# Performance work log

Hardware: AMD Instinct MI355X
Metric: run time of the kernel (lower is better)

The kernel has to match this reference:

```python
import jax, jax.numpy as jnp
import numpy as np

NODE_DIM = 128
NUM_IRREPS = 224          # 128 + 64 + 32 gates (one per irrep channel)
SPH_DIM = 480             # 128*1 + 64*3 + 32*5
HIDDEN = NODE_DIM + 2 * NUM_IRREPS  # 576
NUM_BASIS = 20
N_NODES = 10000
N_EDGES = 160000
# Each gate scalar is broadcast over its irrep's (2l+1) components.
_REPEATS = np.array([1] * 128 + [3] * 64 + [5] * 32)


def _expand_gate(g):
    # [E, 224] -> [E, 480], repeating each gate over its irrep dimension
    return jnp.repeat(g, _REPEATS, axis=-1, total_repeat_length=SPH_DIM)


def setup_inputs() -> dict:
    key = jax.random.key(0)
    ks = jax.random.split(key, 12)
    x_scalar = jax.random.normal(ks[0], (N_NODES, NODE_DIM), dtype=jnp.float32)
    x_spherical = jax.random.normal(ks[1], (N_NODES, SPH_DIM), dtype=jnp.float32)
    rbf = jax.random.uniform(ks[2], (N_EDGES, NUM_BASIS), dtype=jnp.float32)
    fcut = jax.random.uniform(ks[3], (N_EDGES, 1), dtype=jnp.float32)
    rsh = jax.random.normal(ks[4], (N_EDGES, SPH_DIM), dtype=jnp.float32)
    edge_index = jax.random.randint(ks[5], (2, N_EDGES), 0, N_NODES, dtype=jnp.int64)
    s1 = 1.0 / np.sqrt(NODE_DIM)
    s2 = 1.0 / np.sqrt(NUM_BASIS)
    W1 = jax.random.uniform(ks[6], (NODE_DIM, NODE_DIM), jnp.float32, -s1, s1)
    b1 = jnp.zeros((NODE_DIM,), jnp.float32)
    W2 = jax.random.uniform(ks[7], (NODE_DIM, HIDDEN), jnp.float32, -s1, s1)
    b2 = jnp.zeros((HIDDEN,), jnp.float32)
    Wr = jax.random.uniform(ks[8], (NUM_BASIS, HIDDEN), jnp.float32, -s2, s2)
    br = jnp.zeros((HIDDEN,), jnp.float32)
    return {"x_scalar": x_scalar, "x_spherical": x_spherical, "rbf": rbf,
            "fcut": fcut, "rsh": rsh, "edge_index": edge_index,
            "W1": W1, "b1": b1, "W2": W2, "b2": b2, "Wr": Wr, "br": br}


def reference(x_scalar, x_spherical, rbf, fcut, rsh, edge_index,
              W1, b1, W2, b2, Wr, br):
    src, dst = edge_index[0], edge_index[1]
    # scalar MLP: Linear -> SiLU -> Linear
    scalar_out = jax.nn.silu(x_scalar @ W1 + b1) @ W2 + b2          # [N, 576]
    filter_weight = (rbf @ Wr + br) * fcut                          # [E, 576]
    filter_out = scalar_out[dst] * filter_weight                    # [E, 576]
    gate_state = filter_out[:, :NUM_IRREPS]                         # [E, 224]
    gate_edge = filter_out[:, NUM_IRREPS:2 * NUM_IRREPS]            # [E, 224]
    message_scalar = filter_out[:, 2 * NUM_IRREPS:]                 # [E, 128]
    # ElementwiseTensorProduct(edge_irreps, '224x0e'): per-channel scalar gating
    message_spherical = (x_spherical[dst] * _expand_gate(gate_state)
                         + rsh * _expand_gate(gate_edge))           # [E, 480]
    new_scalar = x_scalar.at[src].add(message_scalar)
    new_spherical = x_spherical.at[src].add(message_spherical)
    return (new_scalar, new_spherical)
```

## Files before the change

kernel.cpp:

```cpp
#include <hip/hip_runtime.h>

#define NODE_DIM 128
#define NUM_IRREPS 224
#define SPH_DIM 480
#define HIDDEN 576
#define NUM_BASIS 20
#define N_NODES 10000
#define N_EDGES 160000
#define NPB 4
#define EB 16
#define NT 36
#define IRP 233
#define SCP 138
#define PREP_BLOCKS 2048
#define MLP_BLOCKS ((N_NODES + NPB - 1) / NPB)

typedef __attribute__((ext_vector_type(8))) short short8v;
typedef __attribute__((ext_vector_type(4))) float f32x4;

__device__ __forceinline__ unsigned short f2bf(float f) {
    unsigned int u = __builtin_bit_cast(unsigned int, f);
    u = (u + 0x7fff + ((u >> 16) & 1)) >> 16;
    return (unsigned short)u;
}
__device__ __forceinline__ float bf2f(unsigned short h) {
    unsigned int u = ((unsigned int)h) << 16;
    return __builtin_bit_cast(float, u);
}

__global__ __launch_bounds__(256) void prep_mlp_kernel(
    const float* __restrict__ xs, const float* __restrict__ xsp,
    float* __restrict__ out,
    const int* __restrict__ eidx, int* __restrict__ counts,
    const float* __restrict__ Wr, unsigned short* __restrict__ bfrag,
    const float* __restrict__ W1, const float* __restrict__ b1,
    const float* __restrict__ W2, const float* __restrict__ b2,
    unsigned short* __restrict__ so_bf)
{
    const int t = threadIdx.x;
    if (blockIdx.x < PREP_BLOCKS) {
        const int stride = PREP_BLOCKS * 256;
        const int gt = blockIdx.x * 256 + t;
        for (int i = gt; i < N_NODES * NODE_DIM; i += stride) out[i] = xs[i];
        float* o2 = out + (size_t)N_NODES * NODE_DIM;
        for (int i = gt; i < N_NODES * SPH_DIM; i += stride) o2[i] = xsp[i];
        if (gt < N_EDGES) atomicAdd(&counts[eidx[gt]], 1);
        if (blockIdx.x == PREP_BLOCKS - 1) {
            for (int idx = t; idx < NT * 64; idx += 256) {
                const int nt = idx >> 6, l = idx & 63;
                const int col = nt * 16 + (l & 15);
                const int kb = (l >> 4) * 8;
                #pragma unroll
                for (int j = 0; j < 8; ++j) {
                    const int k = kb + j;
                    bfrag[(size_t)idx * 8 + j] = (k < NUM_BASIS) ? f2bf(Wr[k * HIDDEN + col]) : (unsigned short)0;
                }
            }
        }
        return;
    }
    __shared__ float xsm[NPB][NODE_DIM];
    __shared__ float hsm[NPB][NODE_DIM];
    const int n0 = (blockIdx.x - PREP_BLOCKS) * NPB;
    const int half = t >> 7;
    const int tc = t & 127;

    #pragma unroll
    for (int i = 0; i < 2; ++i) {
        const int nn = 2 * half + i;
        const int node = n0 + nn;
        xsm[nn][tc] = (node < N_NODES) ? xs[(size_t)node * NODE_DIM + tc] : 0.f;
    }
    __syncthreads();

    float acc[2] = {b1[tc], b1[tc]};
    for (int k = 0; k < NODE_DIM; ++k) {
        const float w = W1[k * NODE_DIM + tc];
        #pragma unroll
        for (int i = 0; i < 2; ++i) acc[i] = fmaf(xsm[2 * half + i][k], w, acc[i]);
    }
    #pragma unroll
    for (int i = 0; i < 2; ++i) {
        const float v = acc[i];
        hsm[2 * half + i][tc] = v / (1.f + __expf(-v));
    }
    __syncthreads();

    for (int j = t; j < HIDDEN; j += 256) {
        float a2[NPB];
        #pragma unroll
        for (int n = 0; n < NPB; ++n) a2[n] = b2[j];
        for (int k = 0; k < NODE_DIM; ++k) {
            const float w = W2[k * HIDDEN + j];
            #pragma unroll
            for (int n = 0; n < NPB; ++n) a2[n] = fmaf(hsm[n][k], w, a2[n]);
        }
        #pragma unroll
        for (int n = 0; n < NPB; ++n) {
            const int node = n0 + n;
            if (node < N_NODES) so_bf[(size_t)node * HIDDEN + j] = f2bf(a2[n]);
        }
    }
}

__global__ __launch_bounds__(1024) void scan_kernel(const int* __restrict__ counts,
                                                    int* __restrict__ offsets,
                                                    int* __restrict__ cursor) {
    __shared__ int wsum[16];
    const int tid = threadIdx.x;
    int vals[10];
    int run = 0;
    #pragma unroll
    for (int i = 0; i < 10; ++i) {
        int idx = tid * 10 + i;
        int c = (idx < N_NODES) ? counts[idx] : 0;
        vals[i] = run;
        run += c;
    }
    const int lane = tid & 63, w = tid >> 6;
    int inc = run;
    #pragma unroll
    for (int off = 1; off < 64; off <<= 1) {
        int v = __shfl_up(inc, off);
        if (lane >= off) inc += v;
    }
    if (lane == 63) wsum[w] = inc;
    __syncthreads();
    if (w == 0) {
        int v = (lane < 16) ? wsum[lane] : 0;
        #pragma unroll
        for (int off = 1; off < 16; off <<= 1) {
            int u = __shfl_up(v, off);
            if (lane >= off) v += u;
        }
        if (lane < 16) wsum[lane] = v;
    }
    __syncthreads();
    const int wbase = (w > 0) ? wsum[w - 1] : 0;
    const int base = wbase + inc - run;
    #pragma unroll
    for (int i = 0; i < 10; ++i) {
        int idx = tid * 10 + i;
        if (idx < N_NODES) {
            int v = base + vals[i];
            offsets[idx] = v;
            cursor[idx] = v;
        }
    }
    if (tid == 1023) offsets[N_NODES] = wbase + inc;
}

__global__ __launch_bounds__(256) void scatter_kernel(const int* __restrict__ eidx,
                                                      int* __restrict__ cursor,
                                                      int* __restrict__ edge_order,
                                                      int* __restrict__ edge_src) {
    int i = blockIdx.x * blockDim.x + threadIdx.x;
    if (i < N_EDGES) {
        int s = eidx[i];
        int pos = atomicAdd(&cursor[s], 1);
        edge_order[pos] = i;
        edge_src[pos] = s;
    }
}

__device__ __forceinline__ int gate_of(int d) {
    return (d < 128) ? d : (d < 320) ? (128 + (d - 128) / 3) : (192 + (d - 320) / 5);
}

__global__ __launch_bounds__(256, 4) void edge_mfma(
    const float* __restrict__ xsp,
    const float* __restrict__ rbf, const float* __restrict__ fcut,
    const float* __restrict__ rsh, const int* __restrict__ eidx,
    const unsigned short* __restrict__ bfrag, const float* __restrict__ br,
    const unsigned short* __restrict__ so_bf,
    const int* __restrict__ edge_order, const int* __restrict__ edge_src,
    float* __restrict__ out_scalar, float* __restrict__ out_sph)
{
    __shared__ unsigned int   pair_s[EB][IRP];
    __shared__ unsigned short scal_s[EB][SCP];
    __shared__ int   e_s[EB];
    __shared__ int   src_s[EB];
    __shared__ int   dst_s[EB];
    __shared__ float fc_s[EB];

    const int t = threadIdx.x;
    const int base = blockIdx.x * EB;
    const int lane = t & 63, w = t >> 6;

    const int m_row = lane & 15;
    const int kb = (lane >> 4) * 8;
    const int e_row = edge_order[base + m_row];
    short8v a0;
    {
        const float* rrow = rbf + (size_t)e_row * NUM_BASIS;
        #pragma unroll
        for (int j = 0; j < 8; ++j) {
            const int k = kb + j;
            a0[j] = (k < NUM_BASIS) ? (short)f2bf(rrow[k]) : (short)0;
        }
    }

    if (t < EB) {
        int pos = base + t;
        int e = edge_order[pos];
        e_s[t]   = e;
        src_s[t] = edge_src[pos];
        dst_s[t] = eidx[N_EDGES + e];
        fc_s[t]  = fcut[e];
    }
    __syncthreads();

    {
        const int rbase = (lane >> 4) * 4;
        int   dA[4];
        float fA[4];
        #pragma unroll
        for (int r = 0; r < 4; ++r) { dA[r] = dst_s[rbase + r]; fA[r] = fc_s[rbase + r]; }
        #pragma unroll
        for (int i = 0; i < NT / 4; ++i) {
            const int nt = w * (NT / 4) + i;
            const short8v bf = *(const short8v*)(bfrag + (size_t)(nt * 64 + lane) * 8);
            f32x4 c0 = {0.f, 0.f, 0.f, 0.f};
            c0 = __builtin_amdgcn_mfma_f32_16x16x32_bf16(a0, bf, c0, 0, 0, 0);
            const int col = nt * 16 + (lane & 15);
            const float brc = br[col];
            #pragma unroll
            for (int r = 0; r < 4; ++r) {
                const int row = rbase + r;
                const float sov = bf2f(so_bf[(size_t)dA[r] * HIDDEN + col]);
                const float v = (c0[r] + brc) * fA[r] * sov;
                const unsigned short hv = f2bf(v);
                if (col < NUM_IRREPS) {
                    ((unsigned short*)&pair_s[row][col])[0] = hv;
                } else if (col < 2 * NUM_IRREPS) {
                    ((unsigned short*)&pair_s[row][col - NUM_IRREPS])[1] = hv;
                } else {
                    scal_s[row][col - 2 * NUM_IRREPS] = hv;
                }
            }
        }
    }
    __syncthreads();

    const bool sphOn = (t < 240);
    const int d0 = 2 * t;
    const int g0 = sphOn ? gate_of(d0) : 0;
    const int g1 = sphOn ? gate_of(d0 + 1) : 0;

    float accS = 0.f, accD0 = 0.f, accD1 = 0.f;
    int cur_src = src_s[0];

    float xq0, xq1, rq0, rq1;
    if (sphOn) {
        const float2 xv = *(const float2*)(xsp + (size_t)dst_s[0] * SPH_DIM + d0);
        const float2 rv = *(const float2*)(rsh + (size_t)e_s[0]  * SPH_DIM + d0);
        xq0 = xv.x; xq1 = xv.y; rq0 = rv.x; rq1 = rv.y;
    }

    #pragma unroll
    for (int le = 0; le < EB; ++le) {
        float nx0, nx1, nr0, nr1;
        if (sphOn && le + 1 < EB) {
            const float2 xv = *(const float2*)(xsp + (size_t)dst_s[le + 1] * SPH_DIM + d0);
            const float2 rv = *(const float2*)(rsh + (size_t)e_s[le + 1]  * SPH_DIM + d0);
            nx0 = xv.x; nx1 = xv.y; nr0 = rv.x; nr1 = rv.y;
        }
        const int s = src_s[le];
        if (s != cur_src) {
            if (sphOn) {
                atomicAdd(&out_sph[(size_t)cur_src * SPH_DIM + d0],     accD0);
                atomicAdd(&out_sph[(size_t)cur_src * SPH_DIM + d0 + 1], accD1);
            }
            if (t < 128) atomicAdd(&out_scalar[(size_t)cur_src * NODE_DIM + t], accS);
            accD0 = accD1 = accS = 0.f;
            cur_src = s;
        }
        if (sphOn) {
            const unsigned int p0 = pair_s[le][g0];
            const unsigned int p1 = pair_s[le][g1];
            accD0 = fmaf(xq0, bf2f((unsigned short)(p0 & 0xffffu)),
                    fmaf(rq0, bf2f((unsigned short)(p0 >> 16)), accD0));
            accD1 = fmaf(xq1, bf2f((unsigned short)(p1 & 0xffffu)),
                    fmaf(rq1, bf2f((unsigned short)(p1 >> 16)), accD1));
        }
        if (t < 128) accS += bf2f(scal_s[le][t]);
        if (sphOn && le + 1 < EB) { xq0 = nx0; xq1 = nx1; rq0 = nr0; rq1 = nr1; }
    }
    if (sphOn) {
        atomicAdd(&out_sph[(size_t)cur_src * SPH_DIM + d0],     accD0);
        atomicAdd(&out_sph[(size_t)cur_src * SPH_DIM + d0 + 1], accD1);
    }
    if (t < 128) atomicAdd(&out_scalar[(size_t)cur_src * NODE_DIM + t], accS);
}

extern "C" void kernel_launch(void* const* d_in, const int* in_sizes, int n_in,
                              void* d_out, int out_size, void* d_ws, size_t ws_size,
                              hipStream_t stream) {
    const float* x_scalar    = (const float*)d_in[0];
    const float* x_spherical = (const float*)d_in[1];
    const float* rbf         = (const float*)d_in[2];
    const float* fcut        = (const float*)d_in[3];
    const float* rsh         = (const float*)d_in[4];
    const int*   eidx        = (const int*)d_in[5];
    const float* W1          = (const float*)d_in[6];
    const float* b1          = (const float*)d_in[7];
    const float* W2          = (const float*)d_in[8];
    const float* b2          = (const float*)d_in[9];
    const float* Wr          = (const float*)d_in[10];
    const float* br          = (const float*)d_in[11];

    float* out        = (float*)d_out;
    float* out_scalar = out;
    float* out_sph    = out + (size_t)N_NODES * NODE_DIM;

    unsigned short* so_bf   = (unsigned short*)d_ws;
    int*   counts     = (int*)(so_bf + (size_t)N_NODES * HIDDEN);
    int*   offsets    = counts + N_NODES;
    int*   cursor     = offsets + N_NODES + 1;
    int*   edge_order = cursor + N_NODES;
    int*   edge_src   = edge_order + N_EDGES;
    unsigned short* bfrag = (unsigned short*)((((uintptr_t)(edge_src + N_EDGES)) + 15) & ~(uintptr_t)15);

    hipMemsetAsync(counts, 0, N_NODES * sizeof(int), stream);
    prep_mlp_kernel<<<PREP_BLOCKS + MLP_BLOCKS, 256, 0, stream>>>(
        x_scalar, x_spherical, out, eidx, counts, Wr, bfrag,
        W1, b1, W2, b2, so_bf);
    scan_kernel<<<1, 1024, 0, stream>>>(counts, offsets, cursor);
    scatter_kernel<<<(N_EDGES + 255) / 256, 256, 0, stream>>>(eidx, cursor, edge_order, edge_src);
    edge_mfma<<<N_EDGES / EB, 256, 0, stream>>>(x_spherical, rbf, fcut, rsh, eidx,
                                                bfrag, br, so_bf, edge_order, edge_src,
                                                out_scalar, out_sph);
}
```

Before: 285.1 us.

## Stage gathered scalar_out rows and rbf in LDS before the filter MFMA

```diff
diff --git a/kernel.cpp b/kernel.cpp
--- a/kernel.cpp
+++ b/kernel.cpp
@@ -12,6 +12,7 @@
 #define NT 36
 #define IRP 233
 #define SCP 138
+#define SOP 577
 #define PREP_BLOCKS 2048
 #define MLP_BLOCKS ((N_NODES + NPB - 1) / NPB)
 
@@ -176,8 +177,10 @@
     const int* __restrict__ edge_order, const int* __restrict__ edge_src,
     float* __restrict__ out_scalar, float* __restrict__ out_sph)
 {
+    __shared__ unsigned short so_s[EB][SOP];
     __shared__ unsigned int   pair_s[EB][IRP];
     __shared__ unsigned short scal_s[EB][SCP];
+    __shared__ float rbf_s[EB][NUM_BASIS];
     __shared__ int   e_s[EB];
     __shared__ int   src_s[EB];
     __shared__ int   dst_s[EB];
@@ -186,19 +189,6 @@
     const int t = threadIdx.x;
     const int base = blockIdx.x * EB;
     const int lane = t & 63, w = t >> 6;
-
-    const int m_row = lane & 15;
-    const int kb = (lane >> 4) * 8;
-    const int e_row = edge_order[base + m_row];
-    short8v a0;
-    {
-        const float* rrow = rbf + (size_t)e_row * NUM_BASIS;
-        #pragma unroll
-        for (int j = 0; j < 8; ++j) {
-            const int k = kb + j;
-            a0[j] = (k < NUM_BASIS) ? (short)f2bf(rrow[k]) : (short)0;
-        }
-    }
 
     if (t < EB) {
         int pos = base + t;
@@ -210,12 +200,30 @@
     }
     __syncthreads();
 
+    for (int i = t; i < EB * HIDDEN; i += 256) {
+        const int row = i / HIDDEN, col = i - row * HIDDEN;
+        so_s[row][col] = so_bf[(size_t)dst_s[row] * HIDDEN + col];
+    }
+    for (int i = t; i < EB * NUM_BASIS; i += 256) {
+        const int row = i / NUM_BASIS, k = i - row * NUM_BASIS;
+        rbf_s[row][k] = rbf[(size_t)e_s[row] * NUM_BASIS + k];
+    }
+    __syncthreads();
+
+    const int m_row = lane & 15;
+    const int kb = (lane >> 4) * 8;
+    short8v a0;
+    #pragma unroll
+    for (int j = 0; j < 8; ++j) {
+        const int k = kb + j;
+        a0[j] = (k < NUM_BASIS) ? (short)f2bf(rbf_s[m_row][k]) : (short)0;
+    }
+
     {
         const int rbase = (lane >> 4) * 4;
-        int   dA[4];
         float fA[4];
         #pragma unroll
-        for (int r = 0; r < 4; ++r) { dA[r] = dst_s[rbase + r]; fA[r] = fc_s[rbase + r]; }
+        for (int r = 0; r < 4; ++r) fA[r] = fc_s[rbase + r];
         #pragma unroll
         for (int i = 0; i < NT / 4; ++i) {
             const int nt = w * (NT / 4) + i;
@@ -227,7 +235,7 @@
             #pragma unroll
             for (int r = 0; r < 4; ++r) {
                 const int row = rbase + r;
-                const float sov = bf2f(so_bf[(size_t)dA[r] * HIDDEN + col]);
+                const float sov = bf2f(so_s[row][col]);
                 const float v = (c0[r] + brc) * fA[r] * sov;
                 const unsigned short hv = f2bf(v);
                 if (col < NUM_IRREPS) {
@@ -250,21 +258,8 @@
     float accS = 0.f, accD0 = 0.f, accD1 = 0.f;
     int cur_src = src_s[0];
 
-    float xq0, xq1, rq0, rq1;
-    if (sphOn) {
-        const float2 xv = *(const float2*)(xsp + (size_t)dst_s[0] * SPH_DIM + d0);
-        const float2 rv = *(const float2*)(rsh + (size_t)e_s[0]  * SPH_DIM + d0);
-        xq0 = xv.x; xq1 = xv.y; rq0 = rv.x; rq1 = rv.y;
-    }
-
     #pragma unroll
     for (int le = 0; le < EB; ++le) {
-        float nx0, nx1, nr0, nr1;
-        if (sphOn && le + 1 < EB) {
-            const float2 xv = *(const float2*)(xsp + (size_t)dst_s[le + 1] * SPH_DIM + d0);
-            const float2 rv = *(const float2*)(rsh + (size_t)e_s[le + 1]  * SPH_DIM + d0);
-            nx0 = xv.x; nx1 = xv.y; nr0 = rv.x; nr1 = rv.y;
-        }
         const int s = src_s[le];
         if (s != cur_src) {
             if (sphOn) {
@@ -276,15 +271,16 @@
             cur_src = s;
         }
         if (sphOn) {
+            const float2 xv = *(const float2*)(xsp + (size_t)dst_s[le] * SPH_DIM + d0);
+            const float2 rv = *(const float2*)(rsh + (size_t)e_s[le]  * SPH_DIM + d0);
             const unsigned int p0 = pair_s[le][g0];
             const unsigned int p1 = pair_s[le][g1];
-            accD0 = fmaf(xq0, bf2f((unsigned short)(p0 & 0xffffu)),
-                    fmaf(rq0, bf2f((unsigned short)(p0 >> 16)), accD0));
-            accD1 = fmaf(xq1, bf2f((unsigned short)(p1 & 0xffffu)),
-                    fmaf(rq1, bf2f((unsigned short)(p1 >> 16)), accD1));
+            accD0 = fmaf(xv.x, bf2f((unsigned short)(p0 & 0xffffu)),
+                    fmaf(rv.x, bf2f((unsigned short)(p0 >> 16)), accD0));
+            accD1 = fmaf(xv.y, bf2f((unsigned short)(p1 & 0xffffu)),
+                    fmaf(rv.y, bf2f((unsigned short)(p1 >> 16)), accD1));
         }
         if (t < 128) accS += bf2f(scal_s[le][t]);
-        if (sphOn && le + 1 < EB) { xq0 = nx0; xq1 = nx1; rq0 = nr0; rq1 = nr1; }
     }
     if (sphOn) {
         atomicAdd(&out_sph[(size_t)cur_src * SPH_DIM + d0],     accD0);
```

Result: slower. 336.0 us (+17.8%).
